# Kernel tuning notes

Measured on AMD Instinct MI355X. Metric: run time of the kernel, lower is better.

Reference implementation:

```python
import jax, jax.numpy as jnp
import numpy as np

D_MODEL = 256
D_INNER = 512   # expand=2
D_STATE = 16
D_CONV = 4
DT_RANK = 16    # ceil(256/16)
N_LAYERS = 4
BATCH = 16
SEQLEN = 1024


def setup_inputs() -> dict:
    key = jax.random.key(0)
    ks = jax.random.split(key, 30)
    rn = lambda k, shape, s=0.02: (jax.random.normal(k, shape, jnp.float32) * s)
    # packet features: proto in [0,255], len, flags in [0,63], iat, dir in {0,1}
    u = jax.random.uniform(ks[0], (BATCH, SEQLEN, 5), jnp.float32)
    x = u * jnp.array([255.0, 1.0, 63.0, 1.0, 1.0], jnp.float32)
    L = N_LAYERS
    inp = {
        'x': x,
        # PacketEmbedder
        'emb_proto': rn(ks[1], (256, 32)),
        'emb_flags': rn(ks[2], (64, 32)),
        'emb_dir': rn(ks[3], (2, 8)),
        'proj_len_w': rn(ks[4], (32, 1)), 'proj_len_b': rn(ks[5], (32,)),
        'proj_iat_w': rn(ks[6], (32, 1)), 'proj_iat_b': rn(ks[7], (32,)),
        'fusion_w': rn(ks[8], (D_MODEL, 136)), 'fusion_b': rn(ks[9], (D_MODEL,)),
        'tok_norm_g': jnp.ones((D_MODEL,)), 'tok_norm_b': jnp.zeros((D_MODEL,)),
        # shared post-block LayerNorm
        'norm_g': jnp.ones((D_MODEL,)), 'norm_b': jnp.zeros((D_MODEL,)),
        # 4 Mamba blocks, params stacked on leading layer dim
        'in_proj_w': rn(ks[10], (L, 2 * D_INNER, D_MODEL)),
        'conv_w': rn(ks[11], (L, D_INNER, D_CONV), 0.1),
        'conv_b': rn(ks[12], (L, D_INNER)),
        'x_proj_w': rn(ks[13], (L, DT_RANK + 2 * D_STATE, D_INNER)),
        'dt_w': rn(ks[14], (L, D_INNER, DT_RANK)),
        'dt_b': rn(ks[15], (L, D_INNER)),
        'A_log': jnp.log(jnp.tile(jnp.arange(1, D_STATE + 1, dtype=jnp.float32)[None, None, :], (L, D_INNER, 1))),
        'D_param': jnp.ones((L, D_INNER)),
        'out_proj_w': rn(ks[16], (L, D_MODEL, D_INNER)),
        # exit classifier '32' (eval mode, dropout = identity)
        'cls_w1': rn(ks[17], (128, D_MODEL)), 'cls_b1': rn(ks[18], (128,)),
        'cls_w2': rn(ks[19], (2, 128)), 'cls_b2': rn(ks[20], (2,)),
    }
    return inp


def _ln(h, g, b):
    m = h.mean(-1, keepdims=True)
    v = ((h - m) ** 2).mean(-1, keepdims=True)
    return (h - m) / jnp.sqrt(v + 1e-5) * g + b


def _mamba(u, ipw, cw, cb, xpw, dtw, dtb, alog, dprm, opw):
    # u: [B, L, D_MODEL]
    xz = u @ ipw.T                                   # [B, L, 2*Di]
    xx, z = jnp.split(xz, 2, axis=-1)
    # causal depthwise conv1d over time
    xt = xx.transpose(0, 2, 1)                       # [B, Di, L]
    xc = jax.lax.conv_general_dilated(
        xt, cw[:, None, :], (1,), [(D_CONV - 1, 0)],
        dimension_numbers=('NCH', 'OIH', 'NCH'), feature_group_count=D_INNER)
    xc = jax.nn.silu(xc + cb[None, :, None]).transpose(0, 2, 1)  # [B, L, Di]
    dbl = xc @ xpw.T                                 # [B, L, dt_rank + 2*N]
    dtr = dbl[..., :DT_RANK]
    Bm = dbl[..., DT_RANK:DT_RANK + D_STATE]         # [B, L, N]
    Cm = dbl[..., DT_RANK + D_STATE:]                # [B, L, N]
    dt = jax.nn.softplus(dtr @ dtw.T + dtb)          # [B, L, Di]
    A = -jnp.exp(alog)                               # [Di, N]

    def step(h, inp):
        dt_t, B_t, C_t, x_t = inp                    # [B,Di],[B,N],[B,N],[B,Di]
        dA = jnp.exp(dt_t[:, :, None] * A)           # [B, Di, N]
        h = dA * h + (dt_t * x_t)[:, :, None] * B_t[:, None, :]
        return h, jnp.einsum('bdn,bn->bd', h, C_t)

    h0 = jnp.zeros((u.shape[0], D_INNER, D_STATE), u.dtype)
    xs = (dt.transpose(1, 0, 2), Bm.transpose(1, 0, 2),
          Cm.transpose(1, 0, 2), xc.transpose(1, 0, 2))
    _, ys = jax.lax.scan(step, h0, xs)               # ys: [L, B, Di]
    y = ys.transpose(1, 0, 2) + dprm * xc
    y = y * jax.nn.silu(z)
    return y @ opw.T                                 # [B, L, D_MODEL]


def reference(x, emb_proto, emb_flags, emb_dir, proj_len_w, proj_len_b,
              proj_iat_w, proj_iat_b, fusion_w, fusion_b, tok_norm_g, tok_norm_b,
              norm_g, norm_b, in_proj_w, conv_w, conv_b, x_proj_w, dt_w, dt_b,
              A_log, D_param, out_proj_w, cls_w1, cls_b1, cls_w2, cls_b2):
    proto = jnp.clip(x[:, :, 0].astype(jnp.int32), 0, 255)
    length = x[:, :, 1:2]
    flags = jnp.clip(x[:, :, 2].astype(jnp.int32), 0, 63)
    iat = x[:, :, 3:4]
    direc = jnp.clip(x[:, :, 4].astype(jnp.int32), 0, 1)
    cat = jnp.concatenate([
        emb_proto[proto],
        length @ proj_len_w.T + proj_len_b,
        emb_flags[flags],
        iat @ proj_iat_w.T + proj_iat_b,
        emb_dir[direc],
    ], axis=-1)                                      # [B, L, 136]
    feat = _ln(cat @ fusion_w.T + fusion_b, tok_norm_g, tok_norm_b)
    for i in range(N_LAYERS):
        y = _mamba(feat, in_proj_w[i], conv_w[i], conv_b[i], x_proj_w[i],
                   dt_w[i], dt_b[i], A_log[i], D_param[i], out_proj_w[i])
        feat = _ln(y + feat, norm_g, norm_b)
    idx = min(32, feat.shape[1]) - 1
    h = feat[:, idx, :]
    h = jax.nn.relu(h @ cls_w1.T + cls_b1)
    return h @ cls_w2.T + cls_b2                     # [B, 2]
```

## Files before the change

kernel.cpp:

```cpp
#include <hip/hip_runtime.h>
#include <cmath>

#define TT 32
#define NTOK 512
#define DM 256
#define DI 512

typedef float vf4 __attribute__((ext_vector_type(4)));

__device__ __forceinline__ float silu_(float x){ return x / (1.f + __expf(-x)); }

#define FMA16() do { \
  acc[0][0] += xv.x*wv.x; acc[0][1] += xv.x*wv.y; acc[0][2] += xv.x*wv.z; acc[0][3] += xv.x*wv.w; \
  acc[1][0] += xv.y*wv.x; acc[1][1] += xv.y*wv.y; acc[1][2] += xv.y*wv.z; acc[1][3] += xv.y*wv.w; \
  acc[2][0] += xv.z*wv.x; acc[2][1] += xv.z*wv.y; acc[2][2] += xv.z*wv.z; acc[2][3] += xv.z*wv.w; \
  acc[3][0] += xv.w*wv.x; acc[3][1] += xv.w*wv.y; acc[3][2] += xv.w*wv.z; acc[3][3] += xv.w*wv.w; \
} while(0)

__global__ __launch_bounds__(128)
void k_front(const float* __restrict__ x,
             const float* __restrict__ ep, const float* __restrict__ ef,
             const float* __restrict__ ed,
             const float* __restrict__ plw, const float* __restrict__ plb,
             const float* __restrict__ piw, const float* __restrict__ pib,
             const float* __restrict__ fw,  const float* __restrict__ fb,
             float* __restrict__ s0)
{
  __shared__ float Xs[136*36];
  __shared__ float Ws[136*68];
  int bb = blockIdx.y;
  int n0 = blockIdx.x*64;
  int tid = threadIdx.x;
  for (int r = 0; r < 34; ++r){
    int idx = r*128 + tid;
    int t = idx & 31, j = idx >> 5;
    const float* xr = x + ((size_t)(bb*1024 + t))*5;
    float v;
    if      (j <  32){ int i = __float2int_rz(xr[0]); i = min(max(i,0),255); v = ep[i*32 + j]; }
    else if (j <  64){ v = xr[1]*plw[j-32] + plb[j-32]; }
    else if (j <  96){ int i = __float2int_rz(xr[2]); i = min(max(i,0),63);  v = ef[i*32 + (j-64)]; }
    else if (j < 128){ v = xr[3]*piw[j-96] + pib[j-96]; }
    else             { int i = __float2int_rz(xr[4]); i = min(max(i,0),1);   v = ed[i*8 + (j-128)]; }
    Xs[j*36 + t] = v;
  }
  {
    int c = tid >> 1, jh = tid & 1;
    const float4* src = (const float4*)(fw + (size_t)(n0 + c)*136 + jh*68);
    #pragma unroll
    for (int q = 0; q < 17; ++q){
      float4 v = src[q];
      int j = jh*68 + q*4;
      Ws[(j+0)*68 + c] = v.x; Ws[(j+1)*68 + c] = v.y;
      Ws[(j+2)*68 + c] = v.z; Ws[(j+3)*68 + c] = v.w;
    }
  }
  __syncthreads();
  int my = tid >> 4, nx = tid & 15;
  float acc[4][4] = {};
  #pragma unroll 4
  for (int k = 0; k < 136; ++k){
    float4 xv = *(const float4*)&Xs[k*36 + my*4];
    float4 wv = *(const float4*)&Ws[k*68 + nx*4];
    FMA16();
  }
  #pragma unroll
  for (int i = 0; i < 4; ++i){
    int t = my*4 + i;
    float4 o;
    o.x = acc[i][0] + fb[n0 + nx*4 + 0];
    o.y = acc[i][1] + fb[n0 + nx*4 + 1];
    o.z = acc[i][2] + fb[n0 + nx*4 + 2];
    o.w = acc[i][3] + fb[n0 + nx*4 + 3];
    *(float4*)&s0[(size_t)(bb*32 + t)*DM + n0 + nx*4] = o;
  }
}

__global__ __launch_bounds__(64)
void k_rln(const float* __restrict__ p0, const float* __restrict__ g,
           const float* __restrict__ b, float* __restrict__ feat)
{
  int p = blockIdx.x, tid = threadIdx.x;
  size_t off = (size_t)p*DM + tid*4;
  float4 v = *(const float4*)&p0[off];
  float s  = v.x + v.y + v.z + v.w;
  float sq = v.x*v.x + v.y*v.y + v.z*v.z + v.w*v.w;
  #pragma unroll
  for (int o = 1; o < 64; o <<= 1){ s += __shfl_xor(s, o, 64); sq += __shfl_xor(sq, o, 64); }
  float mu = s * (1.f/256.f);
  float var = sq * (1.f/256.f) - mu*mu;
  float r = rsqrtf(var + 1e-5f);
  float4 gg = *(const float4*)&g[tid*4];
  float4 bb = *(const float4*)&b[tid*4];
  float4 o;
  o.x = (v.x-mu)*r*gg.x + bb.x;
  o.y = (v.y-mu)*r*gg.y + bb.y;
  o.z = (v.z-mu)*r*gg.z + bb.z;
  o.w = (v.w-mu)*r*gg.w + bb.w;
  *(float4*)&feat[off] = o;
}

__global__ __launch_bounds__(64)
void k_rln16(const float* __restrict__ parts, const float* __restrict__ featIn,
             const float* __restrict__ g, const float* __restrict__ b,
             float* __restrict__ feat)
{
  int p = blockIdx.x, tid = threadIdx.x;
  size_t off = (size_t)p*DM + tid*4;
  float4 v = *(const float4*)&parts[off];
  #pragma unroll
  for (int q = 1; q < 16; ++q){
    float4 a = *(const float4*)&parts[(size_t)q*NTOK*DM + off];
    v.x+=a.x; v.y+=a.y; v.z+=a.z; v.w+=a.w;
  }
  { float4 a = *(const float4*)&featIn[off]; v.x+=a.x; v.y+=a.y; v.z+=a.z; v.w+=a.w; }
  float s  = v.x + v.y + v.z + v.w;
  float sq = v.x*v.x + v.y*v.y + v.z*v.z + v.w*v.w;
  #pragma unroll
  for (int o = 1; o < 64; o <<= 1){ s += __shfl_xor(s, o, 64); sq += __shfl_xor(sq, o, 64); }
  float mu = s * (1.f/256.f);
  float var = sq * (1.f/256.f) - mu*mu;
  float r = rsqrtf(var + 1e-5f);
  float4 gg = *(const float4*)&g[tid*4];
  float4 bb = *(const float4*)&b[tid*4];
  float4 o;
  o.x = (v.x-mu)*r*gg.x + bb.x;
  o.y = (v.y-mu)*r*gg.y + bb.y;
  o.z = (v.z-mu)*r*gg.z + bb.z;
  o.w = (v.w-mu)*r*gg.w + bb.w;
  *(float4*)&feat[off] = o;
}

__global__ __launch_bounds__(512)
void k_A(const float* __restrict__ wip, const float* __restrict__ cwl,
         const float* __restrict__ cbl, const float* __restrict__ xpl,
         const float* __restrict__ feat,
         float* __restrict__ xc, float* __restrict__ zs, float* __restrict__ pxp)
{
  extern __shared__ float lds[];
  float* Xs  = lds;
  float* Ws  = lds + 9216;
  float* sxz = lds + 13568;
  float* xcl = lds + 15648;
  int tid = threadIdx.x;
  int nt = blockIdx.x, b = blockIdx.y;
  int n0 = nt*64;

  {
    int t = tid >> 4, kq = tid & 15;
    const float4* src = (const float4*)(feat + (size_t)(b*32 + t)*DM);
    #pragma unroll
    for (int q = 0; q < 4; ++q){
      float4 v = src[q*16 + kq];
      int k = (q*16 + kq)*4;
      Xs[(k+0)*36 + t] = v.x; Xs[(k+1)*36 + t] = v.y;
      Xs[(k+2)*36 + t] = v.z; Xs[(k+3)*36 + t] = v.w;
    }
  }
  int tg = tid >> 6, cc = tid & 63;
  float a0 = 0.f, a1 = 0.f, a2 = 0.f, a3 = 0.f;
  for (int kc = 0; kc < 4; ++kc){
    __syncthreads();
    {
      int c = tid >> 3, kh = tid & 7;
      const float4* src = (const float4*)(wip + (size_t)(n0+c)*DM + kc*64 + kh*8);
      #pragma unroll
      for (int q = 0; q < 2; ++q){
        float4 v = src[q];
        int k = kh*8 + q*4;
        Ws[(k+0)*68 + c] = v.x; Ws[(k+1)*68 + c] = v.y;
        Ws[(k+2)*68 + c] = v.z; Ws[(k+3)*68 + c] = v.w;
      }
    }
    __syncthreads();
    #pragma unroll 8
    for (int kk = 0; kk < 64; ++kk){
      vf4 xv = *(const vf4*)&Xs[(kc*64 + kk)*36 + tg*4];
      float wv = Ws[kk*68 + cc];
      a0 += xv[0]*wv; a1 += xv[1]*wv; a2 += xv[2]*wv; a3 += xv[3]*wv;
    }
  }
  __syncthreads();
  sxz[(tg*4+0)*65 + cc] = a0;
  sxz[(tg*4+1)*65 + cc] = a1;
  sxz[(tg*4+2)*65 + cc] = a2;
  sxz[(tg*4+3)*65 + cc] = a3;
  __syncthreads();

  {
    int t = tid >> 4, c4 = (tid & 15)*4;
    float rr[4];
    if (n0 < 512){
      #pragma unroll
      for (int j = 0; j < 4; ++j){
        int c = c4 + j, d = n0 + c;
        float4 k4 = *(const float4*)(cwl + (size_t)d*4);
        float a = cbl[d];
        if (t >= 3) a += k4.x*sxz[(t-3)*65 + c];
        if (t >= 2) a += k4.y*sxz[(t-2)*65 + c];
        if (t >= 1) a += k4.z*sxz[(t-1)*65 + c];
        a += k4.w*sxz[t*65 + c];
        rr[j] = silu_(a);
        xcl[t*65 + c] = rr[j];
      }
      float4 o = {rr[0], rr[1], rr[2], rr[3]};
      *(float4*)&xc[(size_t)(b*32 + t)*DI + n0 + c4] = o;
    } else {
      #pragma unroll
      for (int j = 0; j < 4; ++j) rr[j] = silu_(sxz[t*65 + c4 + j]);
      float4 o = {rr[0], rr[1], rr[2], rr[3]};
      *(float4*)&zs[(size_t)(b*32 + t)*DI + (n0 - 512) + c4] = o;
    }
  }
  if (n0 < 512){
    __syncthreads();
    int w = tid >> 6, ln = tid & 63;
    int tt = ln & 31, half = ln >> 5;
    #pragma unroll
    for (int j = 0; j < 6; ++j){
      int c = w*6 + j;
      const float* wr = xpl + (size_t)c*DI + n0 + half*32;
      const float* xr = xcl + tt*65 + half*32;
      float pa = 0.f;
      #pragma unroll 8
      for (int q = 0; q < 32; ++q) pa += wr[q]*xr[q];
      pa += __shfl_xor(pa, 32, 64);
      if (half == 0) pxp[((size_t)(b*8 + nt)*48 + c)*32 + tt] = pa;
    }
  }
}

__global__ __launch_bounds__(512)
void k_sc(const float* __restrict__ pxp,
          const float* __restrict__ dtwl, const float* __restrict__ dtbl,
          const float* __restrict__ alogl, const float* __restrict__ dprl,
          const float* __restrict__ opwl,
          const float* __restrict__ xc, const float* __restrict__ zs,
          float* __restrict__ parts)
{
  __shared__ float sdtr[32*18], sB[32*18], sC[32*18];
  __shared__ float sdt[32*33], sxv[32*33], szz[32*33];
  __shared__ float ygT[32*36];
  __shared__ float Wop[32*260];
  int tid = threadIdx.x;
  int ds = blockIdx.x, b = blockIdx.y;
  int d0 = ds*32;

  #pragma unroll
  for (int r = 0; r < 3; ++r){
    int o = r*512 + tid;
    int c = o >> 5, t = o & 31;
    size_t p0 = ((size_t)(b*8)*48 + c)*32 + t;
    float v = 0.f;
    #pragma unroll
    for (int nb = 0; nb < 8; ++nb) v += pxp[p0 + (size_t)nb*1536];
    if      (c < 16) sdtr[t*18 + c] = v;
    else if (c < 32) sB[t*18 + (c-16)] = v;
    else             sC[t*18 + (c-32)] = v;
  }
  {
    int t = tid >> 4, q = (tid & 15)*2;
    size_t base = (size_t)(b*32 + t)*DI + d0 + q;
    float2 u = *(const float2*)&xc[base];
    float2 w = *(const float2*)&zs[base];
    sxv[t*33 + q] = u.x; sxv[t*33 + q + 1] = u.y;
    szz[t*33 + q] = w.x; szz[t*33 + q + 1] = w.y;
  }
  __syncthreads();
  #pragma unroll
  for (int r = 0; r < 2; ++r){
    int idx = tid*2 + r;
    int t = idx >> 5, dl = idx & 31;
    int d = d0 + dl;
    const float4* dwr = (const float4*)(dtwl + (size_t)d*16);
    float4 w0 = dwr[0], w1 = dwr[1], w2 = dwr[2], w3 = dwr[3];
    const float* sr = &sdtr[t*18];
    float a = dtbl[d];
    a += w0.x*sr[0] + w0.y*sr[1] + w0.z*sr[2] + w0.w*sr[3];
    a += w1.x*sr[4] + w1.y*sr[5] + w1.z*sr[6] + w1.w*sr[7];
    a += w2.x*sr[8] + w2.y*sr[9] + w2.z*sr[10]+ w2.w*sr[11];
    a += w3.x*sr[12]+ w3.y*sr[13]+ w3.z*sr[14]+ w3.w*sr[15];
    sdt[t*33 + dl] = fmaxf(a, 0.f) + log1pf(expf(-fabsf(a)));
  }
  __syncthreads();
  {
    int dd = tid >> 4, nidx = tid & 15;
    int d = d0 + dd;
    float A = -expf(alogl[(size_t)d*16 + nidx]);
    float Dp = dprl[d];
    float h = 0.f;
    #pragma unroll 4
    for (int t = 0; t < TT; ++t){
      float dt = sdt[t*33 + dd];
      float xv = sxv[t*33 + dd];
      h = __expf(dt*A)*h + (dt*xv)*sB[t*18 + nidx];
      float yv = h * sC[t*18 + nidx];
      #pragma unroll
      for (int o = 8; o; o >>= 1) yv += __shfl_xor(yv, o, 64);
      if (nidx == 0) ygT[dd*36 + t] = (yv + Dp*xv) * szz[t*33 + dd];
    }
  }
  __syncthreads();
  {
    int c = tid >> 1, kh = tid & 1;
    const float4* src = (const float4*)(opwl + (size_t)c*DI + d0 + kh*16);
    #pragma unroll
    for (int q = 0; q < 4; ++q){
      float4 v = src[q];
      int k = kh*16 + q*4;
      Wop[(k+0)*260 + c] = v.x; Wop[(k+1)*260 + c] = v.y;
      Wop[(k+2)*260 + c] = v.z; Wop[(k+3)*260 + c] = v.w;
    }
  }
  __syncthreads();
  {
    int w = tid >> 6;
    int cq = (tid & 63)*4;
    float acc[4][4] = {};
    #pragma unroll 4
    for (int k = 0; k < 32; ++k){
      vf4 xv = *(const vf4*)&ygT[k*36 + w*4];
      vf4 wv = *(const vf4*)&Wop[k*260 + cq];
      #pragma unroll
      for (int i = 0; i < 4; ++i){
        #pragma unroll
        for (int j = 0; j < 4; ++j) acc[i][j] += xv[i]*wv[j];
      }
    }
    float* dst = parts + (size_t)ds*NTOK*DM;
    #pragma unroll
    for (int i = 0; i < 4; ++i){
      float4 o = {acc[i][0], acc[i][1], acc[i][2], acc[i][3]};
      *(float4*)&dst[(size_t)(b*32 + w*4 + i)*DM + cq] = o;
    }
  }
}

__global__ __launch_bounds__(128)
void k_cls(const float* __restrict__ feat,
           const float* __restrict__ w1, const float* __restrict__ b1,
           const float* __restrict__ w2, const float* __restrict__ b2,
           float* __restrict__ out)
{
  __shared__ float h[256];
  __shared__ float h1[128];
  int b = blockIdx.x;
  int tid = threadIdx.x;
  const float* fr = feat + ((size_t)(b*TT + 31))*DM;
  h[tid]       = fr[tid];
  h[tid + 128] = fr[tid + 128];
  __syncthreads();
  float a = b1[tid];
  const float* wr = w1 + (size_t)tid*256;
  #pragma unroll 8
  for (int j = 0; j < 256; ++j) a += h[j]*wr[j];
  h1[tid] = fmaxf(a, 0.f);
  __syncthreads();
  if (tid < 2){
    float a2 = b2[tid];
    const float* wr2 = w2 + (size_t)tid*128;
    #pragma unroll 8
    for (int j = 0; j < 128; ++j) a2 += h1[j]*wr2[j];
    out[b*2 + tid] = a2;
  }
}

extern "C" void kernel_launch(void* const* d_in, const int* in_sizes, int n_in,
                              void* d_out, int out_size, void* d_ws, size_t ws_size,
                              hipStream_t stream)
{
  const float* x   = (const float*)d_in[0];
  const float* ep  = (const float*)d_in[1];
  const float* ef  = (const float*)d_in[2];
  const float* ed  = (const float*)d_in[3];
  const float* plw = (const float*)d_in[4];
  const float* plb = (const float*)d_in[5];
  const float* piw = (const float*)d_in[6];
  const float* pib = (const float*)d_in[7];
  const float* fw  = (const float*)d_in[8];
  const float* fb  = (const float*)d_in[9];
  const float* tg  = (const float*)d_in[10];
  const float* tb  = (const float*)d_in[11];
  const float* ng  = (const float*)d_in[12];
  const float* nb  = (const float*)d_in[13];
  const float* ipw = (const float*)d_in[14];
  const float* cw  = (const float*)d_in[15];
  const float* cb  = (const float*)d_in[16];
  const float* xpw = (const float*)d_in[17];
  const float* dtw = (const float*)d_in[18];
  const float* dtb = (const float*)d_in[19];
  const float* alog= (const float*)d_in[20];
  const float* dpr = (const float*)d_in[21];
  const float* opw = (const float*)d_in[22];
  const float* w1  = (const float*)d_in[23];
  const float* b1  = (const float*)d_in[24];
  const float* w2  = (const float*)d_in[25];
  const float* b2  = (const float*)d_in[26];
  (void)in_sizes; (void)n_in; (void)out_size; (void)ws_size;

  float* ws    = (float*)d_ws;
  float* feat  = ws;
  float* s0    = feat + NTOK*DM;
  float* xc    = s0   + NTOK*DM;
  float* zs    = xc   + NTOK*DI;
  float* pxp   = zs   + NTOK*DI;
  float* parts = pxp  + 196608;

  k_front<<<dim3(4,16),128,0,stream>>>(x, ep,ef,ed, plw,plb,piw,pib, fw,fb, s0);
  k_rln<<<NTOK,64,0,stream>>>(s0, tg, tb, feat);

  for (int ly = 0; ly < 4; ++ly){
    k_A<<<dim3(16,16),512,71680,stream>>>(ipw + (size_t)ly*262144,
                                          cw + (size_t)ly*2048, cb + (size_t)ly*512,
                                          xpw + (size_t)ly*24576,
                                          feat, xc, zs, pxp);
    k_sc<<<dim3(16,16),512,0,stream>>>(pxp,
                                       dtw + (size_t)ly*8192, dtb + (size_t)ly*512,
                                       alog + (size_t)ly*8192, dpr + (size_t)ly*512,
                                       opw + (size_t)ly*131072,
                                       xc, zs, parts);
    k_rln16<<<NTOK,64,0,stream>>>(parts, feat, ng, nb, feat);
  }
  k_cls<<<16,128,0,stream>>>(feat, w1, b1, w2, b2, (float*)d_out);
}
```

Measured before the change: 193.2 us.

## Fuse residual LayerNorm into in-proj kernel and widen scan blocks to 128 channels

Removes the standalone LayerNorm kernels. Each k_A block now sums the split-K partials plus the residual, applies LayerNorm for its 32 tokens, and block nt==0 writes the normalized features to a ping-pong buffer. k_sc now processes 128 inner channels per block (4 blocks per batch instead of 16), so there are only 4 partial sums to reduce instead of 16. Each scan thread carries 4 states, and the out-proj weights are loaded in 4 K chunks. The final LayerNorm moves into the classifier kernel. This cuts 4 launches and most of the partial-sum traffic, at the cost of redundant LayerNorm work across the 16 k_A column blocks and fewer, larger k_sc blocks that use more LDS.

```diff
diff --git a/kernel.cpp b/kernel.cpp
--- a/kernel.cpp
+++ b/kernel.cpp
@@ -75,87 +75,78 @@
   }
 }
 
-__global__ __launch_bounds__(64)
-void k_rln(const float* __restrict__ p0, const float* __restrict__ g,
-           const float* __restrict__ b, float* __restrict__ feat)
-{
-  int p = blockIdx.x, tid = threadIdx.x;
-  size_t off = (size_t)p*DM + tid*4;
-  float4 v = *(const float4*)&p0[off];
-  float s  = v.x + v.y + v.z + v.w;
-  float sq = v.x*v.x + v.y*v.y + v.z*v.z + v.w*v.w;
-  #pragma unroll
-  for (int o = 1; o < 64; o <<= 1){ s += __shfl_xor(s, o, 64); sq += __shfl_xor(sq, o, 64); }
-  float mu = s * (1.f/256.f);
-  float var = sq * (1.f/256.f) - mu*mu;
-  float r = rsqrtf(var + 1e-5f);
-  float4 gg = *(const float4*)&g[tid*4];
-  float4 bb = *(const float4*)&b[tid*4];
-  float4 o;
-  o.x = (v.x-mu)*r*gg.x + bb.x;
-  o.y = (v.y-mu)*r*gg.y + bb.y;
-  o.z = (v.z-mu)*r*gg.z + bb.z;
-  o.w = (v.w-mu)*r*gg.w + bb.w;
-  *(float4*)&feat[off] = o;
-}
-
-__global__ __launch_bounds__(64)
-void k_rln16(const float* __restrict__ parts, const float* __restrict__ featIn,
-             const float* __restrict__ g, const float* __restrict__ b,
-             float* __restrict__ feat)
-{
-  int p = blockIdx.x, tid = threadIdx.x;
-  size_t off = (size_t)p*DM + tid*4;
-  float4 v = *(const float4*)&parts[off];
-  #pragma unroll
-  for (int q = 1; q < 16; ++q){
-    float4 a = *(const float4*)&parts[(size_t)q*NTOK*DM + off];
-    v.x+=a.x; v.y+=a.y; v.z+=a.z; v.w+=a.w;
-  }
-  { float4 a = *(const float4*)&featIn[off]; v.x+=a.x; v.y+=a.y; v.z+=a.z; v.w+=a.w; }
-  float s  = v.x + v.y + v.z + v.w;
-  float sq = v.x*v.x + v.y*v.y + v.z*v.z + v.w*v.w;
-  #pragma unroll
-  for (int o = 1; o < 64; o <<= 1){ s += __shfl_xor(s, o, 64); sq += __shfl_xor(sq, o, 64); }
-  float mu = s * (1.f/256.f);
-  float var = sq * (1.f/256.f) - mu*mu;
-  float r = rsqrtf(var + 1e-5f);
-  float4 gg = *(const float4*)&g[tid*4];
-  float4 bb = *(const float4*)&b[tid*4];
-  float4 o;
-  o.x = (v.x-mu)*r*gg.x + bb.x;
-  o.y = (v.y-mu)*r*gg.y + bb.y;
-  o.z = (v.z-mu)*r*gg.z + bb.z;
-  o.w = (v.w-mu)*r*gg.w + bb.w;
-  *(float4*)&feat[off] = o;
-}
-
 __global__ __launch_bounds__(512)
 void k_A(const float* __restrict__ wip, const float* __restrict__ cwl,
          const float* __restrict__ cbl, const float* __restrict__ xpl,
-         const float* __restrict__ feat,
+         const float* __restrict__ g, const float* __restrict__ bb,
+         const float* __restrict__ parts, int four,
+         const float* __restrict__ featIn, float* __restrict__ featOut,
          float* __restrict__ xc, float* __restrict__ zs, float* __restrict__ pxp)
 {
   extern __shared__ float lds[];
-  float* Xs  = lds;
-  float* Ws  = lds + 9216;
-  float* sxz = lds + 13568;
-  float* xcl = lds + 15648;
+  float* featT = lds;
+  float* Ws    = lds + 9216;
+  float* sxz   = lds + 13568;
+  float* xcl   = lds + 15648;
   int tid = threadIdx.x;
   int nt = blockIdx.x, b = blockIdx.y;
   int n0 = nt*64;
 
   {
-    int t = tid >> 4, kq = tid & 15;
-    const float4* src = (const float4*)(feat + (size_t)(b*32 + t)*DM);
-    #pragma unroll
-    for (int q = 0; q < 4; ++q){
-      float4 v = src[q*16 + kq];
-      int k = (q*16 + kq)*4;
-      Xs[(k+0)*36 + t] = v.x; Xs[(k+1)*36 + t] = v.y;
-      Xs[(k+2)*36 + t] = v.z; Xs[(k+3)*36 + t] = v.w;
-    }
-  }
+    int t = tid & 31, ci = tid >> 5;
+    size_t base = (size_t)(b*32 + t)*DM + ci*16;
+    float v[16];
+    {
+      const float4* p0 = (const float4*)(parts + base);
+      #pragma unroll
+      for (int q = 0; q < 4; ++q){
+        float4 u = p0[q];
+        v[q*4+0]=u.x; v[q*4+1]=u.y; v[q*4+2]=u.z; v[q*4+3]=u.w;
+      }
+    }
+    if (four){
+      #pragma unroll
+      for (int p2 = 1; p2 < 4; ++p2){
+        const float4* pq = (const float4*)(parts + (size_t)p2*NTOK*DM + base);
+        #pragma unroll
+        for (int q = 0; q < 4; ++q){
+          float4 u = pq[q];
+          v[q*4+0]+=u.x; v[q*4+1]+=u.y; v[q*4+2]+=u.z; v[q*4+3]+=u.w;
+        }
+      }
+      const float4* pf = (const float4*)(featIn + base);
+      #pragma unroll
+      for (int q = 0; q < 4; ++q){
+        float4 u = pf[q];
+        v[q*4+0]+=u.x; v[q*4+1]+=u.y; v[q*4+2]+=u.z; v[q*4+3]+=u.w;
+      }
+    }
+    float s = 0.f, sq = 0.f;
+    #pragma unroll
+    for (int j = 0; j < 16; ++j){ s += v[j]; sq += v[j]*v[j]; }
+    float* redS = Ws; float* redQ = Ws + 544;
+    redS[t*17 + ci] = s; redQ[t*17 + ci] = sq;
+    __syncthreads();
+    float S = 0.f, Q = 0.f;
+    #pragma unroll
+    for (int k2 = 0; k2 < 16; ++k2){ S += redS[t*17+k2]; Q += redQ[t*17+k2]; }
+    float mu = S*(1.f/256.f), var = Q*(1.f/256.f) - mu*mu;
+    float r = rsqrtf(var + 1e-5f);
+    #pragma unroll
+    for (int j = 0; j < 16; ++j){
+      int c = ci*16 + j;
+      v[j] = (v[j]-mu)*r*g[c] + bb[c];
+      featT[c*36 + t] = v[j];
+    }
+    if (nt == 0){
+      #pragma unroll
+      for (int q = 0; q < 4; ++q){
+        float4 o = {v[q*4+0], v[q*4+1], v[q*4+2], v[q*4+3]};
+        *(float4*)&featOut[base + q*4] = o;
+      }
+    }
+  }
+
   int tg = tid >> 6, cc = tid & 63;
   float a0 = 0.f, a1 = 0.f, a2 = 0.f, a3 = 0.f;
   for (int kc = 0; kc < 4; ++kc){
@@ -165,16 +156,16 @@
       const float4* src = (const float4*)(wip + (size_t)(n0+c)*DM + kc*64 + kh*8);
       #pragma unroll
       for (int q = 0; q < 2; ++q){
-        float4 v = src[q];
+        float4 u = src[q];
         int k = kh*8 + q*4;
-        Ws[(k+0)*68 + c] = v.x; Ws[(k+1)*68 + c] = v.y;
-        Ws[(k+2)*68 + c] = v.z; Ws[(k+3)*68 + c] = v.w;
+        Ws[(k+0)*68 + c] = u.x; Ws[(k+1)*68 + c] = u.y;
+        Ws[(k+2)*68 + c] = u.z; Ws[(k+3)*68 + c] = u.w;
       }
     }
     __syncthreads();
     #pragma unroll 8
     for (int kk = 0; kk < 64; ++kk){
-      vf4 xv = *(const vf4*)&Xs[(kc*64 + kk)*36 + tg*4];
+      vf4 xv = *(const vf4*)&featT[(kc*64 + kk)*36 + tg*4];
       float wv = Ws[kk*68 + cc];
       a0 += xv[0]*wv; a1 += xv[1]*wv; a2 += xv[2]*wv; a3 += xv[3]*wv;
     }
@@ -237,13 +228,18 @@
           const float* __restrict__ xc, const float* __restrict__ zs,
           float* __restrict__ parts)
 {
-  __shared__ float sdtr[32*18], sB[32*18], sC[32*18];
-  __shared__ float sdt[32*33], sxv[32*33], szz[32*33];
-  __shared__ float ygT[32*36];
-  __shared__ float Wop[32*260];
+  extern __shared__ float lds[];
+  float* sdtr = lds;
+  float* sB   = lds + 576;
+  float* sC   = lds + 1152;
+  float* sdt  = lds + 1728;
+  float* sxv  = lds + 5952;
+  float* szz  = lds + 10176;
+  float* ygT  = lds + 14400;
+  float* Wop  = lds + 19008;
   int tid = threadIdx.x;
   int ds = blockIdx.x, b = blockIdx.y;
-  int d0 = ds*32;
+  int d0 = ds*128;
 
   #pragma unroll
   for (int r = 0; r < 3; ++r){
@@ -258,67 +254,82 @@
     else             sC[t*18 + (c-32)] = v;
   }
   {
-    int t = tid >> 4, q = (tid & 15)*2;
-    size_t base = (size_t)(b*32 + t)*DI + d0 + q;
-    float2 u = *(const float2*)&xc[base];
-    float2 w = *(const float2*)&zs[base];
-    sxv[t*33 + q] = u.x; sxv[t*33 + q + 1] = u.y;
-    szz[t*33 + q] = w.x; szz[t*33 + q + 1] = w.y;
-  }
-  __syncthreads();
-  #pragma unroll
-  for (int r = 0; r < 2; ++r){
-    int idx = tid*2 + r;
-    int t = idx >> 5, dl = idx & 31;
+    int t = tid >> 4, dq = (tid & 15)*8;
+    size_t base = (size_t)(b*32 + t)*DI + d0 + dq;
+    float4 u0 = *(const float4*)&xc[base];
+    float4 u1 = *(const float4*)&xc[base + 4];
+    float4 w0 = *(const float4*)&zs[base];
+    float4 w1 = *(const float4*)&zs[base + 4];
+    *(float4*)&sxv[t*132 + dq]     = u0;
+    *(float4*)&sxv[t*132 + dq + 4] = u1;
+    *(float4*)&szz[t*132 + dq]     = w0;
+    *(float4*)&szz[t*132 + dq + 4] = w1;
+  }
+  __syncthreads();
+  {
+    int dl = tid & 127, tg2 = tid >> 7;
     int d = d0 + dl;
     const float4* dwr = (const float4*)(dtwl + (size_t)d*16);
     float4 w0 = dwr[0], w1 = dwr[1], w2 = dwr[2], w3 = dwr[3];
-    const float* sr = &sdtr[t*18];
-    float a = dtbl[d];
-    a += w0.x*sr[0] + w0.y*sr[1] + w0.z*sr[2] + w0.w*sr[3];
-    a += w1.x*sr[4] + w1.y*sr[5] + w1.z*sr[6] + w1.w*sr[7];
-    a += w2.x*sr[8] + w2.y*sr[9] + w2.z*sr[10]+ w2.w*sr[11];
-    a += w3.x*sr[12]+ w3.y*sr[13]+ w3.z*sr[14]+ w3.w*sr[15];
-    sdt[t*33 + dl] = fmaxf(a, 0.f) + log1pf(expf(-fabsf(a)));
-  }
-  __syncthreads();
-  {
-    int dd = tid >> 4, nidx = tid & 15;
+    float bsv = dtbl[d];
+    #pragma unroll
+    for (int tt2 = 0; tt2 < 8; ++tt2){
+      int t = tg2*8 + tt2;
+      const float* sr = &sdtr[t*18];
+      float a = bsv;
+      a += w0.x*sr[0] + w0.y*sr[1] + w0.z*sr[2] + w0.w*sr[3];
+      a += w1.x*sr[4] + w1.y*sr[5] + w1.z*sr[6] + w1.w*sr[7];
+      a += w2.x*sr[8] + w2.y*sr[9] + w2.z*sr[10]+ w2.w*sr[11];
+      a += w3.x*sr[12]+ w3.y*sr[13]+ w3.z*sr[14]+ w3.w*sr[15];
+      sdt[t*132 + dl] = fmaxf(a, 0.f) + log1pf(expf(-fabsf(a)));
+    }
+  }
+  __syncthreads();
+  {
+    int dd = tid >> 2, n4 = (tid & 3)*4;
     int d = d0 + dd;
-    float A = -expf(alogl[(size_t)d*16 + nidx]);
+    float A[4], hh[4];
+    #pragma unroll
+    for (int j = 0; j < 4; ++j){
+      A[j] = -expf(alogl[(size_t)d*16 + n4 + j]);
+      hh[j] = 0.f;
+    }
     float Dp = dprl[d];
-    float h = 0.f;
     #pragma unroll 4
     for (int t = 0; t < TT; ++t){
-      float dt = sdt[t*33 + dd];
-      float xv = sxv[t*33 + dd];
-      h = __expf(dt*A)*h + (dt*xv)*sB[t*18 + nidx];
-      float yv = h * sC[t*18 + nidx];
-      #pragma unroll
-      for (int o = 8; o; o >>= 1) yv += __shfl_xor(yv, o, 64);
-      if (nidx == 0) ygT[dd*36 + t] = (yv + Dp*xv) * szz[t*33 + dd];
-    }
-  }
-  __syncthreads();
-  {
-    int c = tid >> 1, kh = tid & 1;
-    const float4* src = (const float4*)(opwl + (size_t)c*DI + d0 + kh*16);
-    #pragma unroll
-    for (int q = 0; q < 4; ++q){
-      float4 v = src[q];
-      int k = kh*16 + q*4;
-      Wop[(k+0)*260 + c] = v.x; Wop[(k+1)*260 + c] = v.y;
-      Wop[(k+2)*260 + c] = v.z; Wop[(k+3)*260 + c] = v.w;
-    }
-  }
-  __syncthreads();
-  {
-    int w = tid >> 6;
-    int cq = (tid & 63)*4;
-    float acc[4][4] = {};
+      float dt = sdt[t*132 + dd];
+      float xv = sxv[t*132 + dd];
+      float dx = dt*xv;
+      float yv = 0.f;
+      #pragma unroll
+      for (int j = 0; j < 4; ++j){
+        hh[j] = __expf(dt*A[j])*hh[j] + dx*sB[t*18 + n4 + j];
+        yv += hh[j]*sC[t*18 + n4 + j];
+      }
+      yv += __shfl_xor(yv, 1, 64);
+      yv += __shfl_xor(yv, 2, 64);
+      if (n4 == 0) ygT[dd*36 + t] = (yv + Dp*xv) * szz[t*132 + dd];
+    }
+  }
+  int cW = tid >> 1, khW = tid & 1;
+  int w = tid >> 6, cq = (tid & 63)*4;
+  float acc[4][4] = {};
+  for (int kc = 0; kc < 4; ++kc){
+    __syncthreads();
+    {
+      const float4* src = (const float4*)(opwl + (size_t)cW*DI + d0 + kc*32 + khW*16);
+      #pragma unroll
+      for (int q = 0; q < 4; ++q){
+        float4 u = src[q];
+        int k = khW*16 + q*4;
+        Wop[(k+0)*260 + cW] = u.x; Wop[(k+1)*260 + cW] = u.y;
+        Wop[(k+2)*260 + cW] = u.z; Wop[(k+3)*260 + cW] = u.w;
+      }
+    }
+    __syncthreads();
     #pragma unroll 4
     for (int k = 0; k < 32; ++k){
-      vf4 xv = *(const vf4*)&ygT[k*36 + w*4];
+      vf4 xv = *(const vf4*)&ygT[(kc*32 + k)*36 + w*4];
       vf4 wv = *(const vf4*)&Wop[k*260 + cq];
       #pragma unroll
       for (int i = 0; i < 4; ++i){
@@ -326,34 +337,53 @@
         for (int j = 0; j < 4; ++j) acc[i][j] += xv[i]*wv[j];
       }
     }
-    float* dst = parts + (size_t)ds*NTOK*DM;
-    #pragma unroll
-    for (int i = 0; i < 4; ++i){
-      float4 o = {acc[i][0], acc[i][1], acc[i][2], acc[i][3]};
-      *(float4*)&dst[(size_t)(b*32 + w*4 + i)*DM + cq] = o;
-    }
+  }
+  float* dst = parts + (size_t)ds*NTOK*DM;
+  #pragma unroll
+  for (int i = 0; i < 4; ++i){
+    float4 o = {acc[i][0], acc[i][1], acc[i][2], acc[i][3]};
+    *(float4*)&dst[(size_t)(b*32 + w*4 + i)*DM + cq] = o;
   }
 }
 
 __global__ __launch_bounds__(128)
-void k_cls(const float* __restrict__ feat,
+void k_cls(const float* __restrict__ feat3, const float* __restrict__ parts,
+           const float* __restrict__ ng, const float* __restrict__ nb,
            const float* __restrict__ w1, const float* __restrict__ b1,
            const float* __restrict__ w2, const float* __restrict__ b2,
            float* __restrict__ out)
 {
   __shared__ float h[256];
   __shared__ float h1[128];
-  int b = blockIdx.x;
-  int tid = threadIdx.x;
-  const float* fr = feat + ((size_t)(b*TT + 31))*DM;
-  h[tid]       = fr[tid];
-  h[tid + 128] = fr[tid + 128];
-  __syncthreads();
-  float a = b1[tid];
-  const float* wr = w1 + (size_t)tid*256;
-  #pragma unroll 8
-  for (int j = 0; j < 256; ++j) a += h[j]*wr[j];
-  h1[tid] = fmaxf(a, 0.f);
+  int b = blockIdx.x, tid = threadIdx.x;
+  if (tid < 64){
+    int c4 = tid*4;
+    size_t base = (size_t)(b*32 + 31)*DM + c4;
+    float4 v = *(const float4*)&feat3[base];
+    #pragma unroll
+    for (int q = 0; q < 4; ++q){
+      float4 u = *(const float4*)&parts[(size_t)q*NTOK*DM + base];
+      v.x += u.x; v.y += u.y; v.z += u.z; v.w += u.w;
+    }
+    float sm = v.x+v.y+v.z+v.w;
+    float sq = v.x*v.x+v.y*v.y+v.z*v.z+v.w*v.w;
+    #pragma unroll
+    for (int o = 1; o < 64; o <<= 1){ sm += __shfl_xor(sm, o, 64); sq += __shfl_xor(sq, o, 64); }
+    float mu = sm*(1.f/256.f), var = sq*(1.f/256.f) - mu*mu;
+    float r = rsqrtf(var + 1e-5f);
+    h[c4+0] = (v.x-mu)*r*ng[c4+0] + nb[c4+0];
+    h[c4+1] = (v.y-mu)*r*ng[c4+1] + nb[c4+1];
+    h[c4+2] = (v.z-mu)*r*ng[c4+2] + nb[c4+2];
+    h[c4+3] = (v.w-mu)*r*ng[c4+3] + nb[c4+3];
+  }
+  __syncthreads();
+  {
+    float a = b1[tid];
+    const float* wr = w1 + (size_t)tid*256;
+    #pragma unroll 8
+    for (int j = 0; j < 256; ++j) a += h[j]*wr[j];
+    h1[tid] = fmaxf(a, 0.f);
+  }
   __syncthreads();
   if (tid < 2){
     float a2 = b2[tid];
@@ -398,27 +428,32 @@
   (void)in_sizes; (void)n_in; (void)out_size; (void)ws_size;
 
   float* ws    = (float*)d_ws;
-  float* feat  = ws;
-  float* s0    = feat + NTOK*DM;
-  float* xc    = s0   + NTOK*DM;
-  float* zs    = xc   + NTOK*DI;
-  float* pxp   = zs   + NTOK*DI;
-  float* parts = pxp  + 196608;
+  float* s0    = ws;
+  float* fb0   = s0  + NTOK*DM;
+  float* fb1   = fb0 + NTOK*DM;
+  float* parts = fb1 + NTOK*DM;
+  float* pxp   = parts + 4*NTOK*DM;
+  float* xc    = pxp + 196608;
+  float* zs    = xc  + NTOK*DI;
+  float* fbuf[2] = {fb0, fb1};
 
   k_front<<<dim3(4,16),128,0,stream>>>(x, ep,ef,ed, plw,plb,piw,pib, fw,fb, s0);
-  k_rln<<<NTOK,64,0,stream>>>(s0, tg, tb, feat);
 
   for (int ly = 0; ly < 4; ++ly){
-    k_A<<<dim3(16,16),512,71680,stream>>>(ipw + (size_t)ly*262144,
+    const float* gg = ly ? ng : tg;
+    const float* gb = ly ? nb : tb;
+    const float* pin = ly ? parts : s0;
+    const float* fin = ly ? fbuf[(ly+1)&1] : nullptr;
+    k_A<<<dim3(16,16),512,70912,stream>>>(ipw + (size_t)ly*262144,
                                           cw + (size_t)ly*2048, cb + (size_t)ly*512,
                                           xpw + (size_t)ly*24576,
-                                          feat, xc, zs, pxp);
-    k_sc<<<dim3(16,16),512,0,stream>>>(pxp,
-                                       dtw + (size_t)ly*8192, dtb + (size_t)ly*512,
-                                       alog + (size_t)ly*8192, dpr + (size_t)ly*512,
-                                       opw + (size_t)ly*131072,
-                                       xc, zs, parts);
-    k_rln16<<<NTOK,64,0,stream>>>(parts, feat, ng, nb, feat);
-  }
-  k_cls<<<16,128,0,stream>>>(feat, w1, b1, w2, b2, (float*)d_out);
+                                          gg, gb, pin, ly ? 1 : 0, fin,
+                                          fbuf[ly&1], xc, zs, pxp);
+    k_sc<<<dim3(4,16),512,109312,stream>>>(pxp,
+                                           dtw + (size_t)ly*8192, dtb + (size_t)ly*512,
+                                           alog + (size_t)ly*8192, dpr + (size_t)ly*512,
+                                           opw + (size_t)ly*131072,
+                                           xc, zs, parts);
+  }
+  k_cls<<<16,128,0,stream>>>(fbuf[1], parts, ng, nb, w1, b1, w2, b2, (float*)d_out);
 }
```

Result: slower. 227.0 us (+17.5%).
